# Performance work log

Measured on AMD Instinct MI355X. Metric: run time of the kernel, lower is better.

## Reference

```python
import jax, jax.numpy as jnp
import numpy as np

B, T, V, D = 16, 200, 25, 128
N_Q, N_E = 4, 1024
BETA, ALPHA, SLOPE, LN_EPS = 0.25, 0.1, 0.2, 1e-5

def _ring_adjacency(v):
    A = np.zeros((v, v), dtype=np.float32)
    for i in range(v):
        A[i, (i + 1) % v] = 1.0
        A[i, (i - 1) % v] = 1.0
    A = A + np.eye(v, dtype=np.float32)  # A + I, as in module
    d_inv_sqrt = 1.0 / np.sqrt(A.sum(1))
    return (d_inv_sqrt[:, None] * A) * d_inv_sqrt[None, :]

def setup_inputs() -> dict:
    key = jax.random.key(0)
    k_z, k_e, k_w = jax.random.split(key, 3)
    z = jax.random.normal(k_z, (B, T, V, D), dtype=jnp.float32)
    # xavier_uniform for each [n_e, e_dim] codebook
    lim = float(np.sqrt(6.0 / (N_E + D)))
    emb = jax.random.uniform(k_e, (N_Q, N_E, D), dtype=jnp.float32, minval=-lim, maxval=lim)
    wlim = float(np.sqrt(1.0 / D))
    gcn_w = jax.random.uniform(k_w, (D, D), dtype=jnp.float32, minval=-wlim, maxval=wlim)
    return {
        "z": z,
        "emb": emb,
        "A_norm": jnp.asarray(_ring_adjacency(V)),
        "gcn_w": gcn_w,
        "gcn_b": jnp.zeros((D,), jnp.float32),
        "ln_scale": jnp.ones((D,), jnp.float32),
        "ln_bias": jnp.zeros((D,), jnp.float32),
    }

def _gcn_refine(residual, A_norm, gcn_w, gcn_b, ln_scale, ln_bias):
    # residual: [N, V, d]
    neigh = jnp.einsum('vw,nwd->nvd', A_norm, residual)
    neigh = neigh @ gcn_w.T + gcn_b                      # nn.Linear
    neigh = jnp.where(neigh >= 0, neigh, SLOPE * neigh)  # LeakyReLU(0.2)
    mu = neigh.mean(-1, keepdims=True)
    var = ((neigh - mu) ** 2).mean(-1, keepdims=True)
    neigh = (neigh - mu) / jnp.sqrt(var + LN_EPS) * ln_scale + ln_bias
    return residual + ALPHA * neigh

def reference(z, emb, A_norm, gcn_w, gcn_b, ln_scale, ln_bias):
    b, t, v, d = z.shape
    n_q = emb.shape[0]
    zf = z.reshape(b * t, v, d)
    residual = zf
    cum = jnp.zeros_like(zf)
    losses, idxs = [], []
    for k in range(n_q):
        refined = _gcn_refine(residual, A_norm, gcn_w, gcn_b, ln_scale, ln_bias)
        W = emb[k]                               # [n_e, d]
        flat = refined.reshape(-1, d)            # [N*V, d]
        dist = ((flat ** 2).sum(1, keepdims=True)
                - 2.0 * flat @ W.T
                + (W ** 2).sum(1)[None, :])
        idx = jnp.argmin(dist, axis=1)           # [N*V]
        q = W[idx].reshape(b * t, v, d)          # == one_hot @ W
        # commit and codebook terms are identical squared errors -> (1+beta)*mse
        diff = q - jax.lax.stop_gradient(residual)
        losses.append((1.0 + BETA) * (diff ** 2).mean(-1))
        cum = cum + q
        residual = residual - q
        idxs.append(idx.reshape(b * t, v))
    zq = zf + jax.lax.stop_gradient(cum - zf)    # straight-through
    total_loss = jnp.stack(losses, 0).mean()
    indices = jnp.stack(idxs, -1).reshape(b, t, v, n_q)
    return zq.reshape(b, t, v, d), total_loss, indices
```

## Files before the change

kernel.cpp:

```cpp
#include <hip/hip_runtime.h>

#define ZQ_N    10240000
#define IDX_OFF 10240001
#define FLT_BIG 3.402823466e38f

typedef _Float16 f16x8 __attribute__((ext_vector_type(8)));
typedef float    f32x4 __attribute__((ext_vector_type(4)));

__global__ __launch_bounds__(256) void k_wsq(const float* __restrict__ emb,
                                             float* __restrict__ wsq,
                                             float* __restrict__ loss_part) {
    int t = threadIdx.x;
    int g = blockIdx.x * 256 + t;
    if (g < 1024) loss_part[g] = 0.f;
    int row = blockIdx.x * 64 + (t >> 2);
    int seg = t & 3;
    const float4* p = (const float4*)(emb + row * 128 + seg * 32);
    float a = 0.f;
#pragma unroll
    for (int i = 0; i < 8; i++) {
        float4 w = p[i];
        a = fmaf(w.x, w.x, a); a = fmaf(w.y, w.y, a);
        a = fmaf(w.z, w.z, a); a = fmaf(w.w, w.w, a);
    }
    a += __shfl_xor(a, 1);
    a += __shfl_xor(a, 2);
    if (seg == 0) wsq[row] = a;
}

__global__ __launch_bounds__(256) void k_wsplit(const float* __restrict__ emb,
        _Float16* __restrict__ wh, _Float16* __restrict__ wl,
        const float* __restrict__ gw,
        _Float16* __restrict__ gh, _Float16* __restrict__ gl) {
    int c = blockIdx.x * 256 + threadIdx.x;
    int q   = c >> 14;
    int col = (c >> 4) & 1023;
    int k8  = (c & 15) * 8;
    const float* srcp = emb + q * 131072 + col * 128 + k8;
    float4 a = *(const float4*)(srcp);
    float4 b = *(const float4*)(srcp + 4);
    float vv[8] = {a.x, a.y, a.z, a.w, b.x, b.y, b.z, b.w};
    union { _Float16 h[8]; uint4 u4; } ph, pl;
#pragma unroll
    for (int j = 0; j < 8; j++) {
        float v = vv[j] * 1024.f;
        _Float16 h = (_Float16)v;
        float r1 = v - (float)h;
        ph.h[j] = h; pl.h[j] = (_Float16)r1;
    }
    int P  = col >> 7, w = (col >> 5) & 3, ct = (col >> 4) & 1, lm = col & 15;
    int ks = k8 >> 5, quad = (k8 >> 3) & 3;
    int off = (((P * 4 + w) * 4 + ks) * 2 + ct) * 512 + (quad * 16 + lm) * 8;
    *(uint4*)(wh + q * 131072 + off) = ph.u4;
    *(uint4*)(wl + q * 131072 + off) = pl.u4;

    if (c < 16384) {
        float v = gw[c] * 1024.f;
        _Float16 h = (_Float16)v;
        float r1 = v - (float)h;
        gh[c] = h; gl[c] = (_Float16)r1;
    }
}

__global__ __launch_bounds__(256) void k_refine(const float* __restrict__ zbase,
        const float* __restrict__ emb, const float* __restrict__ idx_f, int stage,
        float* __restrict__ refined, float* __restrict__ s_out,
        const float* __restrict__ An,
        const _Float16* __restrict__ gh, const _Float16* __restrict__ gl,
        const float* __restrict__ gb, const float* __restrict__ lsc,
        const float* __restrict__ lbi) {
    __shared__ __align__(16) float Rn[25 * 128];
    __shared__ __align__(16) unsigned char nbuf[2 * 32 * 136 * 2];
    __shared__ float Al[625];
    __shared__ int cds[75];
    _Float16* nh = (_Float16*)nbuf;
    _Float16* nl = (_Float16*)(nbuf + 8704);
    float*    nei = (float*)nbuf;
    const int tid = threadIdx.x;
    const int n = blockIdx.x;

    if (tid < 75) {
        int r = tid / 3, j = tid - r * 3;
        if (j < stage) cds[tid] = (int)idx_f[(n * 25 + r) * 4 + j];
    }
    for (int i = tid; i < 625; i += 256) Al[i] = An[i];
    __syncthreads();

    const float4* zp = (const float4*)(zbase + n * 3200);
    float4* Rn4 = (float4*)Rn;
    for (int i = tid; i < 800; i += 256) {
        float4 rv = zp[i];
        int r = i >> 5, c4 = (i & 31) * 4;
#pragma unroll
        for (int j = 0; j < 3; j++) {
            if (j < stage) {
                const float4 q = *(const float4*)(emb + j * 131072 + cds[r * 3 + j] * 128 + c4);
                rv.x -= q.x; rv.y -= q.y; rv.z -= q.z; rv.w -= q.w;
            }
        }
        Rn4[i] = rv;
    }
    __syncthreads();

    for (int i = tid; i < 512; i += 256) {
        int r = i >> 4, k8 = (i & 15) * 8;
        union { _Float16 h[8]; uint4 u4; } ph, pl;
        if (r < 25) {
            int vm = (r == 0) ? 24 : r - 1;
            int vp = (r == 24) ? 0 : r + 1;
            float am = Al[r * 25 + vm], a0 = Al[r * 25 + r], ap = Al[r * 25 + vp];
#pragma unroll
            for (int j = 0; j < 8; j++) {
                int d = k8 + j;
                float val = am * Rn[vm * 128 + d];
                val = fmaf(a0, Rn[r  * 128 + d], val);
                val = fmaf(ap, Rn[vp * 128 + d], val);
                float v1 = val * 1024.f;
                _Float16 h = (_Float16)v1; float fh = (float)h;
                ph.h[j] = h; pl.h[j] = (_Float16)(v1 - fh);
            }
        } else {
            ph.u4 = make_uint4(0u, 0u, 0u, 0u);
            pl.u4 = make_uint4(0u, 0u, 0u, 0u);
        }
        int off = r * 136 + k8;
        *(uint4*)(&nh[off]) = ph.u4;
        *(uint4*)(&nl[off]) = pl.u4;
    }
    __syncthreads();

    {
        const int lane = tid & 63;
        const int wv   = tid >> 6;
        const int quad = lane >> 4;
        const int lm   = lane & 15;
        const int bbase = (wv * 32 + lm) * 128 + quad * 8;
        const int abase = lm * 136 + quad * 8;

        f32x4 racc[2][2];
#pragma unroll
        for (int a = 0; a < 2; a++)
#pragma unroll
            for (int b = 0; b < 2; b++) racc[a][b] = (f32x4){0.f, 0.f, 0.f, 0.f};

#pragma unroll
        for (int k0 = 0; k0 < 4; k0++) {
            const int ko = k0 * 32;
            f16x8 ah[2], al[2];
#pragma unroll
            for (int mt = 0; mt < 2; mt++) {
                ah[mt] = *(const f16x8*)(&nh[abase + mt * (16 * 136) + ko]);
                al[mt] = *(const f16x8*)(&nl[abase + mt * (16 * 136) + ko]);
            }
            f16x8 bh[2], bl[2];
#pragma unroll
            for (int ct = 0; ct < 2; ct++) {
                bh[ct] = *(const f16x8*)(gh + bbase + ct * (16 * 128) + ko);
                bl[ct] = *(const f16x8*)(gl + bbase + ct * (16 * 128) + ko);
            }
#pragma unroll
            for (int ct = 0; ct < 2; ct++)
#pragma unroll
                for (int mt = 0; mt < 2; mt++)
                    racc[ct][mt] = __builtin_amdgcn_mfma_f32_16x16x32_f16(ah[mt], bh[ct], racc[ct][mt], 0, 0, 0);
#pragma unroll
            for (int ct = 0; ct < 2; ct++)
#pragma unroll
                for (int mt = 0; mt < 2; mt++)
                    racc[ct][mt] = __builtin_amdgcn_mfma_f32_16x16x32_f16(ah[mt], bl[ct], racc[ct][mt], 0, 0, 0);
#pragma unroll
            for (int ct = 0; ct < 2; ct++)
#pragma unroll
                for (int mt = 0; mt < 2; mt++)
                    racc[ct][mt] = __builtin_amdgcn_mfma_f32_16x16x32_f16(al[mt], bh[ct], racc[ct][mt], 0, 0, 0);
        }

        __syncthreads();

#pragma unroll
        for (int ct = 0; ct < 2; ct++)
#pragma unroll
            for (int mt = 0; mt < 2; mt++)
#pragma unroll
                for (int rg = 0; rg < 4; rg++) {
                    int row = mt * 16 + quad * 4 + rg;
                    if (row < 25)
                        nei[row * 132 + wv * 32 + ct * 16 + lm] =
                            racc[ct][mt][rg] * 9.5367431640625e-07f;
                }
    }
    __syncthreads();

    const int dpg = tid & 31;
    const int vs  = tid >> 5;
    const int dp0 = dpg * 4;

    float4 b4  = *(const float4*)(gb + dp0);
    float4 sc4 = *(const float4*)(lsc + dp0);
    float4 bi4 = *(const float4*)(lbi + dp0);
    const float bb[4] = {b4.x, b4.y, b4.z, b4.w};
    const float sc[4] = {sc4.x, sc4.y, sc4.z, sc4.w};
    const float bi[4] = {bi4.x, bi4.y, bi4.z, bi4.w};

#pragma unroll
    for (int i = 0; i < 4; i++) {
        int v = vs + 8 * i;
        if (v >= 25) break;
        float4 y4 = *(const float4*)(&nei[v * 132 + dp0]);
        const float yin[4] = {y4.x, y4.y, y4.z, y4.w};
        float y[4];
#pragma unroll
        for (int c = 0; c < 4; c++) {
            float t = yin[c] + bb[c];
            y[c] = (t >= 0.f) ? t : 0.2f * t;
        }
        float s1 = y[0] + y[1] + y[2] + y[3];
#pragma unroll
        for (int m = 1; m <= 16; m <<= 1) s1 += __shfl_xor(s1, m);
        float mu = s1 * (1.f / 128.f);
        float d2 = 0.f;
#pragma unroll
        for (int c = 0; c < 4; c++) { float t = y[c] - mu; d2 = fmaf(t, t, d2); }
#pragma unroll
        for (int m = 1; m <= 16; m <<= 1) d2 += __shfl_xor(d2, m);
        float inv = 1.f / sqrtf(d2 * (1.f / 128.f) + 1e-5f);

        float4 rn4 = *(const float4*)(&Rn[v * 128 + dp0]);
        const float rn[4] = {rn4.x, rn4.y, rn4.z, rn4.w};
        float o[4];
#pragma unroll
        for (int c = 0; c < 4; c++)
            o[c] = rn[c] + 0.1f * ((y[c] - mu) * inv * sc[c] + bi[c]);

        *(float4*)(refined + (n * 25 + v) * 128 + dp0) =
            make_float4(o[0], o[1], o[2], o[3]);

        float ss = 0.f;
#pragma unroll
        for (int c = 0; c < 4; c++) ss = fmaf(o[c], o[c], ss);
#pragma unroll
        for (int m = 1; m <= 16; m <<= 1) ss += __shfl_xor(ss, m);
        if (dpg == 0) s_out[n * 25 + v] = ss;
    }
}


#define XPAD 140

#define VQ_LOADB(BH, BL, IT) do {                                              \
    const int _o = ((((IT) >> 2) * 4 + w) * 4 + ((IT) & 3)) * 1024 + lane * 8; \
    BH[0] = *(const f16x8*)(wh + _o);        BL[0] = *(const f16x8*)(wl + _o);        \
    BH[1] = *(const f16x8*)(wh + _o + 512);  BL[1] = *(const f16x8*)(wl + _o + 512);  \
} while (0)

#define VQ_STEP(IT, BH, BL) do {                                               \
    const int _ko = abase + ((IT) & 3) * 32;                                   \
    f16x8 _ah[4], _al[4];                                                      \
    _Pragma("unroll")                                                          \
    for (int _rt = 0; _rt < 4; _rt++) {                                        \
        const int _off = _ko + _rt * (16 * XPAD);                              \
        _ah[_rt] = *(const f16x8*)(&xh_s[_off]);                               \
        _al[_rt] = *(const f16x8*)(&xl_s[_off]);                               \
    }                                                                          \
    _Pragma("unroll")                                                          \
    for (int _ct = 0; _ct < 2; _ct++)                                          \
        _Pragma("unroll")                                                      \
        for (int _rt = 0; _rt < 4; _rt++)                                      \
            acc[_ct][_rt] = __builtin_amdgcn_mfma_f32_16x16x32_f16(_ah[_rt], BH[_ct], acc[_ct][_rt], 0, 0, 0); \
    _Pragma("unroll")                                                          \
    for (int _ct = 0; _ct < 2; _ct++)                                          \
        _Pragma("unroll")                                                      \
        for (int _rt = 0; _rt < 4; _rt++)                                      \
            acc[_ct][_rt] = __builtin_amdgcn_mfma_f32_16x16x32_f16(_ah[_rt], BL[_ct], acc[_ct][_rt], 0, 0, 0); \
    _Pragma("unroll")                                                          \
    for (int _ct = 0; _ct < 2; _ct++)                                          \
        _Pragma("unroll")                                                      \
        for (int _rt = 0; _rt < 4; _rt++)                                      \
            acc[_ct][_rt] = __builtin_amdgcn_mfma_f32_16x16x32_f16(_al[_rt], BH[_ct], acc[_ct][_rt], 0, 0, 0); \
} while (0)

#define VQ_EPI(P) do {                                                         \
    float _sr[16];                                                             \
    _Pragma("unroll")                                                          \
    for (int _rt = 0; _rt < 4; _rt++) {                                        \
        float4 _t = *(const float4*)(s_g + row0 + _rt * 16 + quad * 4);        \
        _sr[_rt * 4 + 0] = _t.x; _sr[_rt * 4 + 1] = _t.y;                      \
        _sr[_rt * 4 + 2] = _t.z; _sr[_rt * 4 + 3] = _t.w;                      \
    }                                                                          \
    _Pragma("unroll")                                                          \
    for (int _ct = 0; _ct < 2; _ct++) {                                        \
        const int _col = (P) * 128 + w * 32 + _ct * 16 + lm;                   \
        const float _wq = wsq_k[_col];                                         \
        _Pragma("unroll")                                                      \
        for (int _rt = 0; _rt < 4; _rt++) {                                    \
            _Pragma("unroll")                                                  \
            for (int _rg = 0; _rg < 4; _rg++) {                                \
                float _d = (_sr[_rt * 4 + _rg]                                 \
                            - 1.9073486328125e-06f * acc[_ct][_rt][_rg]) + _wq;\
                int _s = _rt * 4 + _rg;                                        \
                if (_d < bestv[_s]) { bestv[_s] = _d; besti[_s] = _col; }      \
            }                                                                  \
        }                                                                      \
    }                                                                          \
} while (0)

__global__ __launch_bounds__(256) void k_vq(const float* __restrict__ refined,
        const _Float16* __restrict__ wh,
        const _Float16* __restrict__ wl,
        const float* __restrict__ wsq_k,
        const float* __restrict__ s_g,
        float* __restrict__ idx_out, int stage) {
    __shared__ __align__(16) _Float16 xh_s[64 * XPAD];
    __shared__ __align__(16) _Float16 xl_s[64 * XPAD];
    const int tid = threadIdx.x;
    const int row0 = blockIdx.x * 64;

    const int lane = tid & 63;
    const int w    = tid >> 6;
    const int quad = lane >> 4;
    const int lm   = lane & 15;

    const int abase = lm * XPAD + quad * 8;

    f16x8 bha[2], bla[2], bhb[2], blb[2];
    VQ_LOADB(bha, bla, 0);

    for (int i = tid; i < 1024; i += 256) {
        int r = i >> 4, k8 = (i & 15) * 8;
        const float* srcp = refined + (row0 + r) * 128 + k8;
        float4 a = *(const float4*)(srcp);
        float4 b = *(const float4*)(srcp + 4);
        float vv[8] = {a.x, a.y, a.z, a.w, b.x, b.y, b.z, b.w};
        union { _Float16 h[8]; uint4 u4; } ph, pl;
#pragma unroll
        for (int j = 0; j < 8; j++) {
            float v = vv[j] * 1024.f;
            _Float16 h = (_Float16)v; float fh = (float)h;
            float r1 = v - fh;
            ph.h[j] = h; pl.h[j] = (_Float16)r1;
        }
        int off = r * XPAD + k8;
        *(uint4*)(&xh_s[off]) = ph.u4;
        *(uint4*)(&xl_s[off]) = pl.u4;
    }
    __syncthreads();

    float bestv[16];
    int   besti[16];
#pragma unroll
    for (int s = 0; s < 16; s++) { bestv[s] = FLT_BIG; besti[s] = 0; }

    f32x4 acc[2][4];

#pragma unroll
    for (int ith = 0; ith < 16; ith++) {
        const int it0 = ith * 2, it1 = it0 + 1;
        VQ_LOADB(bhb, blb, it1);
        if ((it0 & 3) == 0) {
#pragma unroll
            for (int a = 0; a < 2; a++)
#pragma unroll
                for (int b = 0; b < 4; b++) acc[a][b] = (f32x4){0.f, 0.f, 0.f, 0.f};
        }
        VQ_STEP(it0, bha, bla);
        if (it1 < 31) VQ_LOADB(bha, bla, it1 + 1);
        VQ_STEP(it1, bhb, blb);
        if ((it1 & 3) == 3) VQ_EPI(it1 >> 2);
    }

#pragma unroll
    for (int s = 0; s < 16; s++) {
#pragma unroll
        for (int m = 1; m <= 8; m <<= 1) {
            float ov = __shfl_xor(bestv[s], m);
            int   oi = __shfl_xor(besti[s], m);
            if (ov < bestv[s] || (ov == bestv[s] && oi < besti[s])) {
                bestv[s] = ov; besti[s] = oi;
            }
        }
    }

    __syncthreads();
    float* redv = (float*)xh_s;
    int*   redi = (int*)xl_s;
    if (lm == 0) {
#pragma unroll
        for (int s = 0; s < 16; s++) {
            int row = (s >> 2) * 16 + quad * 4 + (s & 3);
            redv[w * 64 + row] = bestv[s];
            redi[w * 64 + row] = besti[s];
        }
    }
    __syncthreads();
    if (tid < 64) {
        float bv = redv[tid]; int bi = redi[tid];
#pragma unroll
        for (int ww = 1; ww < 4; ww++) {
            float v2 = redv[ww * 64 + tid]; int i2 = redi[ww * 64 + tid];
            if (v2 < bv || (v2 == bv && i2 < bi)) { bv = v2; bi = i2; }
        }
        idx_out[(row0 + tid) * 4 + stage] = (float)bi;
    }
}

#define FIN_STAGE(K, ACC) do {                                                 \
    const float4 q = *(const float4*)(emb + (K) * 131072 + codes[r * 4 + (K)] * 128 + c4); \
    float dx = q.x - rv.x, dy = q.y - rv.y, dz = q.z - rv.z, dw = q.w - rv.w;  \
    ACC = fmaf(dx, dx, ACC); ACC = fmaf(dy, dy, ACC);                          \
    ACC = fmaf(dz, dz, ACC); ACC = fmaf(dw, dw, ACC);                          \
    s4.x += q.x; s4.y += q.y; s4.z += q.z; s4.w += q.w;                        \
    rv.x -= q.x; rv.y -= q.y; rv.z -= q.z; rv.w -= q.w;                        \
} while (0)

__global__ __launch_bounds__(256) void k_final(const float* __restrict__ z,
        const float* __restrict__ emb, const float* __restrict__ idx_f,
        float* __restrict__ zq, float* __restrict__ loss_part) {
    __shared__ int codes[256];
    const int tid = threadIdx.x;
    const int row0 = blockIdx.x * 64;
    codes[tid] = (int)idx_f[row0 * 4 + tid];
    __syncthreads();

    const float4* zp = (const float4*)(z + row0 * 128);
    float4* zqp = (float4*)(zq + row0 * 128);
    float a0 = 0.f, a1 = 0.f, a2 = 0.f, a3 = 0.f;
#pragma unroll
    for (int j = 0; j < 8; j++) {
        int idx4 = tid + j * 256;
        int r = idx4 >> 5;
        int c4 = (idx4 & 31) * 4;
        float4 rv = zp[idx4];
        float4 s4 = make_float4(0.f, 0.f, 0.f, 0.f);
        FIN_STAGE(0, a0);
        FIN_STAGE(1, a1);
        FIN_STAGE(2, a2);
        FIN_STAGE(3, a3);
        zqp[idx4] = s4;
    }
#pragma unroll
    for (int m = 1; m <= 32; m <<= 1) {
        a0 += __shfl_xor(a0, m); a1 += __shfl_xor(a1, m);
        a2 += __shfl_xor(a2, m); a3 += __shfl_xor(a3, m);
    }
    if ((tid & 63) == 0) {
        float* slot = &loss_part[blockIdx.x & 1023];
        atomicAdd(slot, a0); atomicAdd(slot, a1);
        atomicAdd(slot, a2); atomicAdd(slot, a3);
    }
}

__global__ __launch_bounds__(256) void k_loss(const float* __restrict__ loss_part,
                                              float* __restrict__ out) {
    int t = threadIdx.x;
    float a = loss_part[t] + loss_part[t + 256] + loss_part[t + 512] + loss_part[t + 768];
#pragma unroll
    for (int m = 1; m <= 32; m <<= 1) a += __shfl_xor(a, m);
    __shared__ float w[4];
    if ((t & 63) == 0) w[t >> 6] = a;
    __syncthreads();
    if (t == 0) {
        float s = w[0] + w[1] + w[2] + w[3];
        out[ZQ_N] = s * (1.25f / (128.f * 320000.f));
    }
}

extern "C" void kernel_launch(void* const* d_in, const int* in_sizes, int n_in,
                              void* d_out, int out_size, void* d_ws, size_t ws_size,
                              hipStream_t stream) {
    (void)in_sizes; (void)n_in; (void)out_size; (void)ws_size;
    const float* z   = (const float*)d_in[0];
    const float* emb = (const float*)d_in[1];
    const float* An  = (const float*)d_in[2];
    const float* gw  = (const float*)d_in[3];
    const float* gb  = (const float*)d_in[4];
    const float* lsc = (const float*)d_in[5];
    const float* lbi = (const float*)d_in[6];

    float* out     = (float*)d_out;
    float* zq      = out;
    float* idx_out = out + IDX_OFF;

    float* ws        = (float*)d_ws;
    float* refined   = ws + 10240000;
    _Float16* gh_f16 = (_Float16*)(ws + 20480000);
    _Float16* gl_f16 = (_Float16*)(ws + 20488192);
    _Float16* wh_f16 = (_Float16*)(ws + 20496384);
    _Float16* wl_f16 = (_Float16*)(ws + 20758528);
    float* s_g       = ws + 21020672;
    float* wsq       = ws + 21100672;
    float* loss_part = ws + 21104768;

    k_wsq<<<64, 256, 0, stream>>>(emb, wsq, loss_part);
    k_wsplit<<<256, 256, 0, stream>>>(emb, wh_f16, wl_f16, gw, gh_f16, gl_f16);
    for (int k = 0; k < 4; k++) {
        k_refine<<<3200, 256, 0, stream>>>(z, emb, idx_out, k,
                                           refined, s_g, An,
                                           gh_f16, gl_f16, gb, lsc, lbi);
        k_vq<<<1250, 256, 0, stream>>>(refined,
                                       wh_f16 + k * 131072, wl_f16 + k * 131072,
                                       wsq + k * 1024,
                                       s_g, idx_out, k);
    }
    k_final<<<1250, 256, 0, stream>>>(z, emb, idx_out, zq, loss_part);
    k_loss<<<1, 256, 0, stream>>>(loss_part, out);
}
```

Baseline: 712.8 us.

## Split VQ codebook columns across eight waves per block instead of four

The VQ distance kernel now launches 512 threads per block. Each of the 8 waves owns a contiguous 128-column slice of the codebook and computes one 16-column tile per panel, where before 4 waves each computed two tiles. The codebook split kernel rewrites the fp16 hi/lo layout to match the new per-wave access pattern, and the final argmin reduction now spans 8 waves. The aim is more waves per block and fewer accumulator registers per wave, to improve latency hiding. In exchange, each wave reads the same activation fragments from LDS for half as many MFMAs, so LDS traffic per unit of compute doubles.

```diff
diff --git a/kernel.cpp b/kernel.cpp
--- a/kernel.cpp
+++ b/kernel.cpp
@@ -48,9 +48,9 @@
         float r1 = v - (float)h;
         ph.h[j] = h; pl.h[j] = (_Float16)r1;
     }
-    int P  = col >> 7, w = (col >> 5) & 3, ct = (col >> 4) & 1, lm = col & 15;
+    int w  = col >> 7, p = (col >> 4) & 7, lm = col & 15;
     int ks = k8 >> 5, quad = (k8 >> 3) & 3;
-    int off = (((P * 4 + w) * 4 + ks) * 2 + ct) * 512 + (quad * 16 + lm) * 8;
+    int off = ((w * 8 + p) * 4 + ks) * 512 + (quad * 16 + lm) * 8;
     *(uint4*)(wh + q * 131072 + off) = ph.u4;
     *(uint4*)(wl + q * 131072 + off) = pl.u4;
 
@@ -248,9 +248,9 @@
 #define XPAD 140
 
 #define VQ_LOADB(BH, BL, IT) do {                                              \
-    const int _o = ((((IT) >> 2) * 4 + w) * 4 + ((IT) & 3)) * 1024 + lane * 8; \
-    BH[0] = *(const f16x8*)(wh + _o);        BL[0] = *(const f16x8*)(wl + _o);        \
-    BH[1] = *(const f16x8*)(wh + _o + 512);  BL[1] = *(const f16x8*)(wl + _o + 512);  \
+    const int _o = ((w * 8 + ((IT) >> 2)) * 4 + ((IT) & 3)) * 512 + lane * 8;  \
+    BH = *(const f16x8*)(wh + _o);                                             \
+    BL = *(const f16x8*)(wl + _o);                                             \
 } while (0)
 
 #define VQ_STEP(IT, BH, BL) do {                                               \
@@ -263,20 +263,14 @@
         _al[_rt] = *(const f16x8*)(&xl_s[_off]);                               \
     }                                                                          \
     _Pragma("unroll")                                                          \
-    for (int _ct = 0; _ct < 2; _ct++)                                          \
-        _Pragma("unroll")                                                      \
-        for (int _rt = 0; _rt < 4; _rt++)                                      \
-            acc[_ct][_rt] = __builtin_amdgcn_mfma_f32_16x16x32_f16(_ah[_rt], BH[_ct], acc[_ct][_rt], 0, 0, 0); \
-    _Pragma("unroll")                                                          \
-    for (int _ct = 0; _ct < 2; _ct++)                                          \
-        _Pragma("unroll")                                                      \
-        for (int _rt = 0; _rt < 4; _rt++)                                      \
-            acc[_ct][_rt] = __builtin_amdgcn_mfma_f32_16x16x32_f16(_ah[_rt], BL[_ct], acc[_ct][_rt], 0, 0, 0); \
-    _Pragma("unroll")                                                          \
-    for (int _ct = 0; _ct < 2; _ct++)                                          \
-        _Pragma("unroll")                                                      \
-        for (int _rt = 0; _rt < 4; _rt++)                                      \
-            acc[_ct][_rt] = __builtin_amdgcn_mfma_f32_16x16x32_f16(_al[_rt], BH[_ct], acc[_ct][_rt], 0, 0, 0); \
+    for (int _rt = 0; _rt < 4; _rt++)                                          \
+        acc[_rt] = __builtin_amdgcn_mfma_f32_16x16x32_f16(_ah[_rt], BH, acc[_rt], 0, 0, 0); \
+    _Pragma("unroll")                                                          \
+    for (int _rt = 0; _rt < 4; _rt++)                                          \
+        acc[_rt] = __builtin_amdgcn_mfma_f32_16x16x32_f16(_ah[_rt], BL, acc[_rt], 0, 0, 0); \
+    _Pragma("unroll")                                                          \
+    for (int _rt = 0; _rt < 4; _rt++)                                          \
+        acc[_rt] = __builtin_amdgcn_mfma_f32_16x16x32_f16(_al[_rt], BH, acc[_rt], 0, 0, 0); \
 } while (0)
 
 #define VQ_EPI(P) do {                                                         \
@@ -287,24 +281,21 @@
         _sr[_rt * 4 + 0] = _t.x; _sr[_rt * 4 + 1] = _t.y;                      \
         _sr[_rt * 4 + 2] = _t.z; _sr[_rt * 4 + 3] = _t.w;                      \
     }                                                                          \
-    _Pragma("unroll")                                                          \
-    for (int _ct = 0; _ct < 2; _ct++) {                                        \
-        const int _col = (P) * 128 + w * 32 + _ct * 16 + lm;                   \
-        const float _wq = wsq_k[_col];                                         \
+    const int _col = w * 128 + (P) * 16 + lm;                                  \
+    const float _wq = wsq_k[_col];                                             \
+    _Pragma("unroll")                                                          \
+    for (int _rt = 0; _rt < 4; _rt++) {                                        \
         _Pragma("unroll")                                                      \
-        for (int _rt = 0; _rt < 4; _rt++) {                                    \
-            _Pragma("unroll")                                                  \
-            for (int _rg = 0; _rg < 4; _rg++) {                                \
-                float _d = (_sr[_rt * 4 + _rg]                                 \
-                            - 1.9073486328125e-06f * acc[_ct][_rt][_rg]) + _wq;\
-                int _s = _rt * 4 + _rg;                                        \
-                if (_d < bestv[_s]) { bestv[_s] = _d; besti[_s] = _col; }      \
-            }                                                                  \
+        for (int _rg = 0; _rg < 4; _rg++) {                                    \
+            float _d = (_sr[_rt * 4 + _rg]                                     \
+                        - 1.9073486328125e-06f * acc[_rt][_rg]) + _wq;         \
+            int _s = _rt * 4 + _rg;                                            \
+            if (_d < bestv[_s]) { bestv[_s] = _d; besti[_s] = _col; }          \
         }                                                                      \
     }                                                                          \
 } while (0)
 
-__global__ __launch_bounds__(256) void k_vq(const float* __restrict__ refined,
+__global__ __launch_bounds__(512, 1) void k_vq(const float* __restrict__ refined,
         const _Float16* __restrict__ wh,
         const _Float16* __restrict__ wl,
         const float* __restrict__ wsq_k,
@@ -322,10 +313,10 @@
 
     const int abase = lm * XPAD + quad * 8;
 
-    f16x8 bha[2], bla[2], bhb[2], blb[2];
-    VQ_LOADB(bha, bla, 0);
-
-    for (int i = tid; i < 1024; i += 256) {
+    f16x8 bh_a, bl_a, bh_b, bl_b;
+    VQ_LOADB(bh_a, bl_a, 0);
+
+    for (int i = tid; i < 1024; i += 512) {
         int r = i >> 4, k8 = (i & 15) * 8;
         const float* srcp = refined + (row0 + r) * 128 + k8;
         float4 a = *(const float4*)(srcp);
@@ -350,21 +341,19 @@
 #pragma unroll
     for (int s = 0; s < 16; s++) { bestv[s] = FLT_BIG; besti[s] = 0; }
 
-    f32x4 acc[2][4];
+    f32x4 acc[4];
 
 #pragma unroll
     for (int ith = 0; ith < 16; ith++) {
         const int it0 = ith * 2, it1 = it0 + 1;
-        VQ_LOADB(bhb, blb, it1);
+        VQ_LOADB(bh_b, bl_b, it1);
         if ((it0 & 3) == 0) {
 #pragma unroll
-            for (int a = 0; a < 2; a++)
-#pragma unroll
-                for (int b = 0; b < 4; b++) acc[a][b] = (f32x4){0.f, 0.f, 0.f, 0.f};
-        }
-        VQ_STEP(it0, bha, bla);
-        if (it1 < 31) VQ_LOADB(bha, bla, it1 + 1);
-        VQ_STEP(it1, bhb, blb);
+            for (int b = 0; b < 4; b++) acc[b] = (f32x4){0.f, 0.f, 0.f, 0.f};
+        }
+        VQ_STEP(it0, bh_a, bl_a);
+        if (it1 < 31) VQ_LOADB(bh_a, bl_a, it1 + 1);
+        VQ_STEP(it1, bh_b, bl_b);
         if ((it1 & 3) == 3) VQ_EPI(it1 >> 2);
     }
 
@@ -395,7 +384,7 @@
     if (tid < 64) {
         float bv = redv[tid]; int bi = redi[tid];
 #pragma unroll
-        for (int ww = 1; ww < 4; ww++) {
+        for (int ww = 1; ww < 8; ww++) {
             float v2 = redv[ww * 64 + tid]; int i2 = redi[ww * 64 + tid];
             if (v2 < bv || (v2 == bv && i2 < bi)) { bv = v2; bi = i2; }
         }
@@ -496,7 +485,7 @@
         k_refine<<<3200, 256, 0, stream>>>(z, emb, idx_out, k,
                                            refined, s_g, An,
                                            gh_f16, gl_f16, gb, lsc, lbi);
-        k_vq<<<1250, 256, 0, stream>>>(refined,
+        k_vq<<<1250, 512, 0, stream>>>(refined,
                                        wh_f16 + k * 131072, wl_f16 + k * 131072,
                                        wsq + k * 1024,
                                        s_g, idx_out, k);
```

New measurement: 722.3 us. Within noise of the previous version (+1.3%).
